# Optimization experiments

Measured on AMD Instinct MI355X. Metric: run time of the kernel, lower is better.

The kernel has to match this reference:

```python
import jax, jax.numpy as jnp
import numpy as np

BS, NS, S = 4, 16384, 8
C_PLANE, RES = 64, 128
IN_DIM = 3 * C_PLANE  # 192


def _bilerp(plane, uv):
    """plane: [B,C,H,W]; uv: [B,n,2] in [0,1] -> [B,n,C] bilinear samples (border clamp)."""
    B, C, H, W = plane.shape
    x = jnp.clip(uv[..., 0], 0.0, 1.0) * (W - 1)
    y = jnp.clip(uv[..., 1], 0.0, 1.0) * (H - 1)
    x0 = jnp.floor(x).astype(jnp.int32)
    y0 = jnp.floor(y).astype(jnp.int32)
    x1 = jnp.minimum(x0 + 1, W - 1)
    y1 = jnp.minimum(y0 + 1, H - 1)
    wx = (x - x0)[:, :, None]
    wy = (y - y0)[:, :, None]
    gat = jax.vmap(lambda p, yy, xx: p[:, yy, xx].T)  # per-batch gather -> [n,C]
    f00 = gat(plane, y0, x0)
    f01 = gat(plane, y0, x1)
    f10 = gat(plane, y1, x0)
    f11 = gat(plane, y1, x1)
    return (f00 * (1 - wx) * (1 - wy) + f01 * wx * (1 - wy)
            + f10 * (1 - wx) * wy + f11 * wx * wy)


def _sample_triplane(p, feat_xz, feat_xy, feat_yz):
    """p: [B,n,3] -> concat of bilinear samples from the three planes: [B,n,3C]."""
    f_xz = _bilerp(feat_xz, p[..., jnp.array([0, 2])])
    f_xy = _bilerp(feat_xy, p[..., jnp.array([0, 1])])
    f_yz = _bilerp(feat_yz, p[..., jnp.array([1, 2])])
    return jnp.concatenate([f_xz, f_xy, f_yz], axis=-1)


def setup_inputs() -> dict:
    key = jax.random.key(0)
    ks = jax.random.split(key, 12)
    w = 0.05  # small init so predicted offsets stay near the query point
    return {
        "query_pos": jax.random.uniform(ks[0], (BS, NS, 3), dtype=jnp.float32),
        "feat_xz": jax.random.normal(ks[1], (BS, C_PLANE, RES, RES), dtype=jnp.float32),
        "feat_xy": jax.random.normal(ks[2], (BS, C_PLANE, RES, RES), dtype=jnp.float32),
        "feat_yz": jax.random.normal(ks[3], (BS, C_PLANE, RES, RES), dtype=jnp.float32),
        "W_v": jax.random.normal(ks[4], (IN_DIM, IN_DIM), dtype=jnp.float32) * w,
        "b_v": jnp.zeros((IN_DIM,), jnp.float32),
        "W_out": jax.random.normal(ks[5], (IN_DIM, IN_DIM), dtype=jnp.float32) * w,
        "b_out": jnp.zeros((IN_DIM,), jnp.float32),
        "W_off": jax.random.normal(ks[6], (3 * S, IN_DIM), dtype=jnp.float32) * w,
        "b_off": jnp.zeros((3 * S,), jnp.float32),
        "W_wt": jax.random.normal(ks[7], (S, IN_DIM), dtype=jnp.float32) * w,
        "b_wt": jnp.zeros((S,), jnp.float32),
    }


def reference(query_pos, feat_xz, feat_xy, feat_yz, W_v, b_v, W_out, b_out,
              W_off, b_off, W_wt, b_wt):
    bs, ns, _ = query_pos.shape
    # feature at query points: [bs, ns, IN_DIM]
    feature = _sample_triplane(query_pos, feat_xz, feat_xy, feat_yz)
    # predicted per-sample offsets and weights
    off = (feature @ W_off.T + b_off).reshape(bs, ns, S, 3)
    wt = (feature @ W_wt.T + b_wt)[..., None]            # [bs, ns, S, 1]
    pts = off + query_pos[:, :, None, :]                  # [bs, ns, S, 3]
    # gather features at offset locations: [bs, ns*S, IN_DIM]
    aux = _sample_triplane(pts.reshape(bs, ns * S, 3), feat_xz, feat_xy, feat_yz)
    v = (aux @ W_v.T + b_v).reshape(bs, ns, S, -1)        # [bs, ns, S, hidden]
    out = (v * wt).sum(axis=-2)                           # weighted sum over samples
    out = out @ W_out.T + b_out + feature                 # residual add
    return out  # [bs, ns, IN_DIM]
```

## Files before the change

### kernel.cpp

```cpp
#include <hip/hip_runtime.h>

#define BS 4
#define NS 16384
#define S_SAMP 8
#define CPL 64
#define RES 128
#define IN_DIM 192
#define NPTS (BS * NS)
#define PL_STRIDE (RES * RES * CPL)
#define PLANES_T_FLOATS (BS * 3 * PL_STRIDE)

__global__ __launch_bounds__(256) void transpose_planes(
    const float* __restrict__ xz, const float* __restrict__ xy,
    const float* __restrict__ yz, float* __restrict__ T) {
  __shared__ float tile[64][65];
  int blk = blockIdx.x;
  int xh = blk & 1;
  int y  = (blk >> 1) & 127;
  int pl = (blk >> 8) % 3;
  int b  = blk / 768;
  const float* s = ((pl == 0) ? xz : (pl == 1) ? xy : yz) +
                   (size_t)b * CPL * RES * RES + y * RES + xh * 64;
  int tid = threadIdx.x;
  int xi = tid & 15, c0 = tid >> 4;
#pragma unroll
  for (int r = 0; r < 4; ++r) {
    int c = c0 + r * 16;
    float4 v = *(const float4*)(s + (size_t)c * RES * RES + 4 * xi);
    tile[c][4 * xi + 0] = v.x;
    tile[c][4 * xi + 1] = v.y;
    tile[c][4 * xi + 2] = v.z;
    tile[c][4 * xi + 3] = v.w;
  }
  __syncthreads();
  float* d = T + ((size_t)(b * 3 + pl) * RES * RES + (size_t)y * RES + xh * 64) * CPL;
  int cj = tid & 15, x0 = tid >> 4;
#pragma unroll
  for (int r = 0; r < 4; ++r) {
    int x = x0 + r * 16;
    float4 v;
    v.x = tile[4 * cj + 0][x];
    v.y = tile[4 * cj + 1][x];
    v.z = tile[4 * cj + 2][x];
    v.w = tile[4 * cj + 3][x];
    *(float4*)(d + (size_t)x * CPL + 4 * cj) = v;
  }
}

__global__ __launch_bounds__(192) void precompute_wc(
    const float* __restrict__ W_v, const float* __restrict__ b_v,
    const float* __restrict__ W_out, float* __restrict__ WcT,
    float* __restrict__ bc) {
  int j = blockIdx.x;
  int k = threadIdx.x;
  if (j < IN_DIM) {
    float a0 = 0.f, a1 = 0.f, a2 = 0.f, a3 = 0.f;
#pragma unroll 4
    for (int m = 0; m < IN_DIM; m += 4) {
      a0 += W_out[j * IN_DIM + m + 0] * W_v[(m + 0) * IN_DIM + k];
      a1 += W_out[j * IN_DIM + m + 1] * W_v[(m + 1) * IN_DIM + k];
      a2 += W_out[j * IN_DIM + m + 2] * W_v[(m + 2) * IN_DIM + k];
      a3 += W_out[j * IN_DIM + m + 3] * W_v[(m + 3) * IN_DIM + k];
    }
    WcT[k * IN_DIM + j] = (a0 + a1) + (a2 + a3);
  } else {
    float a0 = 0.f, a1 = 0.f;
#pragma unroll 4
    for (int m = 0; m < IN_DIM; m += 2) {
      a0 += W_out[k * IN_DIM + m] * b_v[m];
      a1 += W_out[k * IN_DIM + m + 1] * b_v[m + 1];
    }
    bc[k] = a0 + a1;
  }
}

__device__ __forceinline__ void coordf(float c, int& i, float& fr) {
  float u = fminf(fmaxf(c, 0.f), 1.f) * 127.f;
  float uf = floorf(u);
  i = (int)uf;
  fr = u - uf;
}

__device__ __forceinline__ float4 bil4(float4 acc, const float* __restrict__ P,
                                       unsigned plBase, int iv, int iu,
                                       float fv, float fu, float wt, int m) {
  unsigned off = plBase + (unsigned)(iv * RES + iu) * CPL + 4u * m;
  unsigned du = (iu < 127) ? CPL : 0u;
  unsigned dv = (iv < 127) ? (unsigned)(RES * CPL) : 0u;
  float4 t0 = *(const float4*)(P + off);
  float4 t1 = *(const float4*)(P + off + du);
  float4 t2 = *(const float4*)(P + off + dv);
  float4 t3 = *(const float4*)(P + off + dv + du);
  float a = wt * (1.f - fu), bq = wt * fu;
  float w0 = a * (1.f - fv), w1 = bq * (1.f - fv), w2 = a * fv, w3 = bq * fv;
  acc.x += t0.x * w0 + t1.x * w1 + t2.x * w2 + t3.x * w3;
  acc.y += t0.y * w0 + t1.y * w1 + t2.y * w2 + t3.y * w3;
  acc.z += t0.z * w0 + t1.z * w1 + t2.z * w2 + t3.z * w3;
  acc.w += t0.w * w0 + t1.w * w1 + t2.w * w2 + t3.w * w3;
  return acc;
}

__global__ __launch_bounds__(256, 4) void fused_sample(
    const float* __restrict__ qpos, const float* __restrict__ planesT,
    const float* __restrict__ W_off, const float* __restrict__ b_off,
    const float* __restrict__ W_wt, const float* __restrict__ b_wt,
    float* __restrict__ waux, float* __restrict__ swtg,
    float* __restrict__ outp) {
  __shared__ float feat_lds[4][IN_DIM];
  __shared__ float offwt[4][32];
  int w = threadIdx.x >> 6, lane = threadIdx.x & 63;
  int q = lane >> 4, m = lane & 15;
  int p = blockIdx.x * 4 + w;
  int b = p >> 14;
  float qx = qpos[p * 3 + 0], qy = qpos[p * 3 + 1], qz = qpos[p * 3 + 2];
  unsigned bOff = (unsigned)b * 3u * PL_STRIDE;

  {
    int ix, iy, iz;
    float fx, fy, fz;
    coordf(qx, ix, fx);
    coordf(qy, iy, fy);
    coordf(qz, iz, fz);
    unsigned off0 = bOff + 0u * PL_STRIDE + (unsigned)(iz * RES + ix) * CPL;
    unsigned off1 = bOff + 1u * PL_STRIDE + (unsigned)(iy * RES + ix) * CPL;
    unsigned off2 = bOff + 2u * PL_STRIDE + (unsigned)(iz * RES + iy) * CPL;
    unsigned du0 = (ix < 127) ? CPL : 0u, dv0 = (iz < 127) ? RES * CPL : 0u;
    unsigned du1 = (ix < 127) ? CPL : 0u, dv1 = (iy < 127) ? RES * CPL : 0u;
    unsigned du2 = (iy < 127) ? CPL : 0u, dv2 = (iz < 127) ? RES * CPL : 0u;
    unsigned offV = (q == 0) ? off0 : (q == 1) ? off1 : off2;
    unsigned duV = (q == 0) ? du0 : (q == 1) ? du1 : du2;
    unsigned dvV = (q == 0) ? dv0 : (q == 1) ? dv1 : dv2;
    float wxV = (q == 0) ? fx : (q == 1) ? fx : fy;
    float wyV = (q == 0) ? fz : (q == 1) ? fy : fz;
    offV += 4u * m;
    float4 t0 = *(const float4*)(planesT + offV);
    float4 t1 = *(const float4*)(planesT + offV + duV);
    float4 t2 = *(const float4*)(planesT + offV + dvV);
    float4 t3 = *(const float4*)(planesT + offV + dvV + duV);
    float cx = 1.f - wxV, cy = 1.f - wyV;
    float w0 = cx * cy, w1 = wxV * cy, w2 = cx * wyV, w3 = wxV * wyV;
    float4 f4;
    f4.x = t0.x * w0 + t1.x * w1 + t2.x * w2 + t3.x * w3;
    f4.y = t0.y * w0 + t1.y * w1 + t2.y * w2 + t3.y * w3;
    f4.z = t0.z * w0 + t1.z * w1 + t2.z * w2 + t3.z * w3;
    f4.w = t0.w * w0 + t1.w * w1 + t2.w * w2 + t3.w * w3;
    if (q < 3) {
      *(float4*)&feat_lds[w][q * 64 + 4 * m] = f4;
      *(float4*)(outp + (size_t)p * IN_DIM + q * 64 + 4 * m) = f4;
    }
  }

  {
    int oj = lane & 31, kh = lane >> 5;
    const float* row = (oj < 24) ? (W_off + oj * IN_DIM)
                                 : (W_wt + (oj - 24) * IN_DIM);
    float bias = (oj < 24) ? b_off[oj] : b_wt[oj - 24];
    const float4* r4 = (const float4*)(row + kh * 96);
    const float4* fl = (const float4*)&feat_lds[w][kh * 96];
    float a0 = 0.f, a1 = 0.f, a2 = 0.f, a3 = 0.f;
#pragma unroll
    for (int k4 = 0; k4 < 24; ++k4) {
      float4 rv = r4[k4];
      float4 fv = fl[k4];
      a0 += rv.x * fv.x;
      a1 += rv.y * fv.y;
      a2 += rv.z * fv.z;
      a3 += rv.w * fv.w;
    }
    float acc = (a0 + a1) + (a2 + a3);
    acc += __shfl_xor(acc, 32);
    if (lane < 32) offwt[w][oj] = acc + bias;
  }

  float4 acc0 = {0, 0, 0, 0}, acc1 = {0, 0, 0, 0}, acc2 = {0, 0, 0, 0};
  float swtA = 0.f;
#pragma unroll
  for (int sb = 0; sb < 2; ++sb) {
    int sl = 4 * sb + q;
    float ox = offwt[w][3 * sl + 0];
    float oy = offwt[w][3 * sl + 1];
    float oz = offwt[w][3 * sl + 2];
    float wt = offwt[w][24 + sl];
    swtA += wt;
    int ix, iy, iz;
    float fx, fy, fz;
    coordf(qx + ox, ix, fx);
    coordf(qy + oy, iy, fy);
    coordf(qz + oz, iz, fz);
    acc0 = bil4(acc0, planesT, bOff + 0u * PL_STRIDE, iz, ix, fz, fx, wt, m);
    acc1 = bil4(acc1, planesT, bOff + 1u * PL_STRIDE, iy, ix, fy, fx, wt, m);
    acc2 = bil4(acc2, planesT, bOff + 2u * PL_STRIDE, iz, iy, fz, fy, wt, m);
  }
#define REDQ(v)                          \
  v.x += __shfl_xor(v.x, 16); v.y += __shfl_xor(v.y, 16); \
  v.z += __shfl_xor(v.z, 16); v.w += __shfl_xor(v.w, 16); \
  v.x += __shfl_xor(v.x, 32); v.y += __shfl_xor(v.y, 32); \
  v.z += __shfl_xor(v.z, 32); v.w += __shfl_xor(v.w, 32);
  REDQ(acc0)
  REDQ(acc1)
  REDQ(acc2)
#undef REDQ
  float4 wv = (q == 0) ? acc0 : (q == 1) ? acc1 : acc2;
  if (q < 3) *(float4*)(waux + (size_t)p * IN_DIM + q * 64 + 4 * m) = wv;
  swtA += __shfl_xor(swtA, 16);
  swtA += __shfl_xor(swtA, 32);
  if (lane == 0) swtg[p] = swtA;
}

__global__ __launch_bounds__(256) void out_gemm(
    const float* __restrict__ waux, const float* __restrict__ swtg,
    const float* __restrict__ WcT, const float* __restrict__ bc,
    const float* __restrict__ b_out, float* __restrict__ out) {
  __shared__ float at[64][193];
  int tid = threadIdx.x;
  int w = tid >> 6, lane = tid & 63;
  int p0 = blockIdx.x * 64;

  const float4* src = (const float4*)(waux + (size_t)p0 * IN_DIM);
#pragma unroll
  for (int i = 0; i < 12; ++i) {
    int idx = tid + i * 256;
    int pp = idx / 48, k4 = idx % 48;
    float4 v = src[idx];
    at[pp][k4 * 4 + 0] = v.x;
    at[pp][k4 * 4 + 1] = v.y;
    at[pp][k4 * 4 + 2] = v.z;
    at[pp][k4 * 4 + 3] = v.w;
  }
  __syncthreads();

  int j0 = __builtin_amdgcn_readfirstlane(w * 48);
  float acc[48] = {};
#pragma unroll 4
  for (int k = 0; k < 192; ++k) {
    float a = at[lane][k];
    const float* wr = WcT + k * IN_DIM + j0;
#pragma unroll
    for (int jj = 0; jj < 48; ++jj) acc[jj] += a * wr[jj];
  }

  int p = p0 + lane;
  float sw = swtg[p];
  size_t ob = (size_t)p * IN_DIM + j0;
#pragma unroll
  for (int g = 0; g < 12; ++g) {
    float4 o = *(const float4*)(out + ob + 4 * g);
    float4 r;
    r.x = acc[4 * g + 0] + sw * bc[j0 + 4 * g + 0] + b_out[j0 + 4 * g + 0] + o.x;
    r.y = acc[4 * g + 1] + sw * bc[j0 + 4 * g + 1] + b_out[j0 + 4 * g + 1] + o.y;
    r.z = acc[4 * g + 2] + sw * bc[j0 + 4 * g + 2] + b_out[j0 + 4 * g + 2] + o.z;
    r.w = acc[4 * g + 3] + sw * bc[j0 + 4 * g + 3] + b_out[j0 + 4 * g + 3] + o.w;
    *(float4*)(out + ob + 4 * g) = r;
  }
}

extern "C" void kernel_launch(void* const* d_in, const int* in_sizes, int n_in,
                              void* d_out, int out_size, void* d_ws,
                              size_t ws_size, hipStream_t stream) {
  const float* qpos  = (const float*)d_in[0];
  const float* xz    = (const float*)d_in[1];
  const float* xy    = (const float*)d_in[2];
  const float* yz    = (const float*)d_in[3];
  const float* W_v   = (const float*)d_in[4];
  const float* b_v   = (const float*)d_in[5];
  const float* W_out = (const float*)d_in[6];
  const float* b_out = (const float*)d_in[7];
  const float* W_off = (const float*)d_in[8];
  const float* b_off = (const float*)d_in[9];
  const float* W_wt  = (const float*)d_in[10];
  const float* b_wt  = (const float*)d_in[11];

  float* ws      = (float*)d_ws;
  float* planesT = ws;
  float* waux    = planesT + PLANES_T_FLOATS;
  float* swtg    = waux + (size_t)NPTS * IN_DIM;
  float* WcT     = swtg + NPTS;
  float* bc      = WcT + IN_DIM * IN_DIM;
  float* out     = (float*)d_out;

  hipLaunchKernelGGL(transpose_planes, dim3(BS * 3 * RES * 2), dim3(256), 0,
                     stream, xz, xy, yz, planesT);
  hipLaunchKernelGGL(precompute_wc, dim3(IN_DIM + 1), dim3(IN_DIM), 0, stream,
                     W_v, b_v, W_out, WcT, bc);
  hipLaunchKernelGGL(fused_sample, dim3(NPTS / 4), dim3(256), 0, stream, qpos,
                     planesT, W_off, b_off, W_wt, b_wt, waux, swtg, out);
  hipLaunchKernelGGL(out_gemm, dim3(NPTS / 64), dim3(256), 0, stream, waux,
                     swtg, WcT, bc, b_out, out);
}
```

Baseline: 480.2 us.

## Split offset gathers into per-plane passes with XCD-aware block mapping, retile out GEMM

The fused sampling kernel is split in two. A feature/offset kernel writes sampled positions and weights to a buffer, and three per-plane gather kernels follow, each touching only one 4 MB plane per batch. Gather blocks are remapped so each XCD handles a single batch, which is meant to keep each plane resident in that XCD's L2 and cut random-gather misses. The output GEMM is also retiled to 32 points per block, with a plain LDS copy and coalesced per-lane weight reads. In exchange it adds extra launches, an offset buffer round-trip, and three separate partial writes to waux.

```diff
diff --git a/kernel.cpp b/kernel.cpp
--- a/kernel.cpp
+++ b/kernel.cpp
@@ -81,30 +81,11 @@
   fr = u - uf;
 }
 
-__device__ __forceinline__ float4 bil4(float4 acc, const float* __restrict__ P,
-                                       unsigned plBase, int iv, int iu,
-                                       float fv, float fu, float wt, int m) {
-  unsigned off = plBase + (unsigned)(iv * RES + iu) * CPL + 4u * m;
-  unsigned du = (iu < 127) ? CPL : 0u;
-  unsigned dv = (iv < 127) ? (unsigned)(RES * CPL) : 0u;
-  float4 t0 = *(const float4*)(P + off);
-  float4 t1 = *(const float4*)(P + off + du);
-  float4 t2 = *(const float4*)(P + off + dv);
-  float4 t3 = *(const float4*)(P + off + dv + du);
-  float a = wt * (1.f - fu), bq = wt * fu;
-  float w0 = a * (1.f - fv), w1 = bq * (1.f - fv), w2 = a * fv, w3 = bq * fv;
-  acc.x += t0.x * w0 + t1.x * w1 + t2.x * w2 + t3.x * w3;
-  acc.y += t0.y * w0 + t1.y * w1 + t2.y * w2 + t3.y * w3;
-  acc.z += t0.z * w0 + t1.z * w1 + t2.z * w2 + t3.z * w3;
-  acc.w += t0.w * w0 + t1.w * w1 + t2.w * w2 + t3.w * w3;
-  return acc;
-}
-
-__global__ __launch_bounds__(256, 4) void fused_sample(
+__global__ __launch_bounds__(256, 4) void feat_off(
     const float* __restrict__ qpos, const float* __restrict__ planesT,
     const float* __restrict__ W_off, const float* __restrict__ b_off,
     const float* __restrict__ W_wt, const float* __restrict__ b_wt,
-    float* __restrict__ waux, float* __restrict__ swtg,
+    float* __restrict__ offpt, float* __restrict__ swtg,
     float* __restrict__ outp) {
   __shared__ float feat_lds[4][IN_DIM];
   __shared__ float offwt[4][32];
@@ -172,85 +153,126 @@
     if (lane < 32) offwt[w][oj] = acc + bias;
   }
 
-  float4 acc0 = {0, 0, 0, 0}, acc1 = {0, 0, 0, 0}, acc2 = {0, 0, 0, 0};
-  float swtA = 0.f;
+  if (lane < 32) {
+    int s = lane >> 2, e = lane & 3;
+    float val;
+    if (e == 3) {
+      val = offwt[w][24 + s];
+    } else {
+      float qc = (e == 0) ? qx : (e == 1) ? qy : qz;
+      val = qc + offwt[w][3 * s + e];
+    }
+    offpt[(size_t)p * 32 + lane] = val;
+  }
+  if (lane == 0) {
+    float sw = 0.f;
+#pragma unroll
+    for (int s = 0; s < S_SAMP; ++s) sw += offwt[w][24 + s];
+    swtg[p] = sw;
+  }
+}
+
+template <int PL>
+__global__ __launch_bounds__(256, 8) void gather_pass(
+    const float* __restrict__ offpt, const float* __restrict__ planesT,
+    float* __restrict__ waux) {
+  int w = threadIdx.x >> 6, lane = threadIdx.x & 63;
+  int q = lane >> 4, m = lane & 15;
+  int i = blockIdx.x;
+  int xcd = i & 7, j = i >> 3;
+  int b = xcd >> 1;
+  int pblk = (xcd & 1) * 2048 + j;
+  int p = b * NS + pblk * 4 + w;
+  const float* P = planesT + ((size_t)b * 3 + PL) * PL_STRIDE;
+  const float4* sp = (const float4*)(offpt + (size_t)p * 32);
+
+  float4 acc = {0.f, 0.f, 0.f, 0.f};
 #pragma unroll
   for (int sb = 0; sb < 2; ++sb) {
-    int sl = 4 * sb + q;
-    float ox = offwt[w][3 * sl + 0];
-    float oy = offwt[w][3 * sl + 1];
-    float oz = offwt[w][3 * sl + 2];
-    float wt = offwt[w][24 + sl];
-    swtA += wt;
-    int ix, iy, iz;
-    float fx, fy, fz;
-    coordf(qx + ox, ix, fx);
-    coordf(qy + oy, iy, fy);
-    coordf(qz + oz, iz, fz);
-    acc0 = bil4(acc0, planesT, bOff + 0u * PL_STRIDE, iz, ix, fz, fx, wt, m);
-    acc1 = bil4(acc1, planesT, bOff + 1u * PL_STRIDE, iy, ix, fy, fx, wt, m);
-    acc2 = bil4(acc2, planesT, bOff + 2u * PL_STRIDE, iz, iy, fz, fy, wt, m);
-  }
-#define REDQ(v)                          \
-  v.x += __shfl_xor(v.x, 16); v.y += __shfl_xor(v.y, 16); \
-  v.z += __shfl_xor(v.z, 16); v.w += __shfl_xor(v.w, 16); \
-  v.x += __shfl_xor(v.x, 32); v.y += __shfl_xor(v.y, 32); \
-  v.z += __shfl_xor(v.z, 32); v.w += __shfl_xor(v.w, 32);
-  REDQ(acc0)
-  REDQ(acc1)
-  REDQ(acc2)
-#undef REDQ
-  float4 wv = (q == 0) ? acc0 : (q == 1) ? acc1 : acc2;
-  if (q < 3) *(float4*)(waux + (size_t)p * IN_DIM + q * 64 + 4 * m) = wv;
-  swtA += __shfl_xor(swtA, 16);
-  swtA += __shfl_xor(swtA, 32);
-  if (lane == 0) swtg[p] = swtA;
+    float4 s4 = sp[q + sb * 4];
+    float u = (PL == 0) ? s4.x : (PL == 1) ? s4.x : s4.y;
+    float v = (PL == 0) ? s4.z : (PL == 1) ? s4.y : s4.z;
+    int iu, iv;
+    float fu, fv;
+    coordf(u, iu, fu);
+    coordf(v, iv, fv);
+    unsigned off = (unsigned)(iv * RES + iu) * CPL + 4u * m;
+    unsigned du = (iu < 127) ? CPL : 0u;
+    unsigned dv = (iv < 127) ? (unsigned)(RES * CPL) : 0u;
+    float4 t0 = *(const float4*)(P + off);
+    float4 t1 = *(const float4*)(P + off + du);
+    float4 t2 = *(const float4*)(P + off + dv);
+    float4 t3 = *(const float4*)(P + off + dv + du);
+    float wt = s4.w;
+    float a = wt * (1.f - fu), bq = wt * fu;
+    float w0 = a * (1.f - fv), w1 = bq * (1.f - fv), w2 = a * fv, w3 = bq * fv;
+    acc.x += t0.x * w0 + t1.x * w1 + t2.x * w2 + t3.x * w3;
+    acc.y += t0.y * w0 + t1.y * w1 + t2.y * w2 + t3.y * w3;
+    acc.z += t0.z * w0 + t1.z * w1 + t2.z * w2 + t3.z * w3;
+    acc.w += t0.w * w0 + t1.w * w1 + t2.w * w2 + t3.w * w3;
+  }
+  acc.x += __shfl_xor(acc.x, 16); acc.y += __shfl_xor(acc.y, 16);
+  acc.z += __shfl_xor(acc.z, 16); acc.w += __shfl_xor(acc.w, 16);
+  acc.x += __shfl_xor(acc.x, 32); acc.y += __shfl_xor(acc.y, 32);
+  acc.z += __shfl_xor(acc.z, 32); acc.w += __shfl_xor(acc.w, 32);
+  if (q == 0)
+    *(float4*)(waux + (size_t)p * IN_DIM + PL * 64 + 4 * m) = acc;
 }
 
 __global__ __launch_bounds__(256) void out_gemm(
     const float* __restrict__ waux, const float* __restrict__ swtg,
     const float* __restrict__ WcT, const float* __restrict__ bc,
     const float* __restrict__ b_out, float* __restrict__ out) {
-  __shared__ float at[64][193];
+  __shared__ float at[32 * IN_DIM];
   int tid = threadIdx.x;
   int w = tid >> 6, lane = tid & 63;
-  int p0 = blockIdx.x * 64;
+  int p0 = blockIdx.x * 32;
 
   const float4* src = (const float4*)(waux + (size_t)p0 * IN_DIM);
-#pragma unroll
-  for (int i = 0; i < 12; ++i) {
-    int idx = tid + i * 256;
-    int pp = idx / 48, k4 = idx % 48;
-    float4 v = src[idx];
-    at[pp][k4 * 4 + 0] = v.x;
-    at[pp][k4 * 4 + 1] = v.y;
-    at[pp][k4 * 4 + 2] = v.z;
-    at[pp][k4 * 4 + 3] = v.w;
-  }
+  float4* dst4 = (float4*)at;
+#pragma unroll
+  for (int i = 0; i < 6; ++i) dst4[tid + i * 256] = src[tid + i * 256];
   __syncthreads();
 
-  int j0 = __builtin_amdgcn_readfirstlane(w * 48);
-  float acc[48] = {};
-#pragma unroll 4
-  for (int k = 0; k < 192; ++k) {
-    float a = at[lane][k];
-    const float* wr = WcT + k * IN_DIM + j0;
-#pragma unroll
-    for (int jj = 0; jj < 48; ++jj) acc[jj] += a * wr[jj];
-  }
-
-  int p = p0 + lane;
-  float sw = swtg[p];
-  size_t ob = (size_t)p * IN_DIM + j0;
-#pragma unroll
-  for (int g = 0; g < 12; ++g) {
-    float4 o = *(const float4*)(out + ob + 4 * g);
-    float4 r;
-    r.x = acc[4 * g + 0] + sw * bc[j0 + 4 * g + 0] + b_out[j0 + 4 * g + 0] + o.x;
-    r.y = acc[4 * g + 1] + sw * bc[j0 + 4 * g + 1] + b_out[j0 + 4 * g + 1] + o.y;
-    r.z = acc[4 * g + 2] + sw * bc[j0 + 4 * g + 2] + b_out[j0 + 4 * g + 2] + o.z;
-    r.w = acc[4 * g + 3] + sw * bc[j0 + 4 * g + 3] + b_out[j0 + 4 * g + 3] + o.w;
-    *(float4*)(out + ob + 4 * g) = r;
+  int pw = w * 8;
+  float acc[8][3] = {};
+#pragma unroll 2
+  for (int k4 = 0; k4 < 48; ++k4) {
+    float v0[4], v1[4], v2[4];
+#pragma unroll
+    for (int kk = 0; kk < 4; ++kk) {
+      const float* r = WcT + (k4 * 4 + kk) * IN_DIM;
+      v0[kk] = r[lane];
+      v1[kk] = r[64 + lane];
+      v2[kk] = r[128 + lane];
+    }
+    float4 a[8];
+#pragma unroll
+    for (int qq = 0; qq < 8; ++qq)
+      a[qq] = *(const float4*)&at[(pw + qq) * IN_DIM + k4 * 4];
+#pragma unroll
+    for (int qq = 0; qq < 8; ++qq) {
+      acc[qq][0] += v0[0] * a[qq].x + v0[1] * a[qq].y + v0[2] * a[qq].z + v0[3] * a[qq].w;
+      acc[qq][1] += v1[0] * a[qq].x + v1[1] * a[qq].y + v1[2] * a[qq].z + v1[3] * a[qq].w;
+      acc[qq][2] += v2[0] * a[qq].x + v2[1] * a[qq].y + v2[2] * a[qq].z + v2[3] * a[qq].w;
+    }
+  }
+
+  float bcv[3], bov[3];
+#pragma unroll
+  for (int t = 0; t < 3; ++t) {
+    bcv[t] = bc[lane + t * 64];
+    bov[t] = b_out[lane + t * 64];
+  }
+#pragma unroll
+  for (int qq = 0; qq < 8; ++qq) {
+    int p = p0 + pw + qq;
+    float sw = swtg[p];
+#pragma unroll
+    for (int t = 0; t < 3; ++t) {
+      size_t o = (size_t)p * IN_DIM + lane + t * 64;
+      out[o] = acc[qq][t] + sw * bcv[t] + bov[t] + out[o];
+    }
   }
 }
 
@@ -273,7 +295,8 @@
   float* ws      = (float*)d_ws;
   float* planesT = ws;
   float* waux    = planesT + PLANES_T_FLOATS;
-  float* swtg    = waux + (size_t)NPTS * IN_DIM;
+  float* offpt   = waux + (size_t)NPTS * IN_DIM;
+  float* swtg    = offpt + (size_t)NPTS * 32;
   float* WcT     = swtg + NPTS;
   float* bc      = WcT + IN_DIM * IN_DIM;
   float* out     = (float*)d_out;
@@ -282,8 +305,14 @@
                      stream, xz, xy, yz, planesT);
   hipLaunchKernelGGL(precompute_wc, dim3(IN_DIM + 1), dim3(IN_DIM), 0, stream,
                      W_v, b_v, W_out, WcT, bc);
-  hipLaunchKernelGGL(fused_sample, dim3(NPTS / 4), dim3(256), 0, stream, qpos,
-                     planesT, W_off, b_off, W_wt, b_wt, waux, swtg, out);
-  hipLaunchKernelGGL(out_gemm, dim3(NPTS / 64), dim3(256), 0, stream, waux,
+  hipLaunchKernelGGL(feat_off, dim3(NPTS / 4), dim3(256), 0, stream, qpos,
+                     planesT, W_off, b_off, W_wt, b_wt, offpt, swtg, out);
+  hipLaunchKernelGGL(gather_pass<0>, dim3(NPTS / 4), dim3(256), 0, stream,
+                     offpt, planesT, waux);
+  hipLaunchKernelGGL(gather_pass<1>, dim3(NPTS / 4), dim3(256), 0, stream,
+                     offpt, planesT, waux);
+  hipLaunchKernelGGL(gather_pass<2>, dim3(NPTS / 4), dim3(256), 0, stream,
+                     offpt, planesT, waux);
+  hipLaunchKernelGGL(out_gemm, dim3(NPTS / 32), dim3(256), 0, stream, waux,
                      swtg, WcT, bc, b_out, out);
 }
```

Measured after the change: 479.2 us. About the same (-0.2%).
